# Performance work log

Measured on AMD Instinct MI355X. Metric: run time of the kernel, lower is better.

## Reference

```python
import jax, jax.numpy as jnp
import numpy as np

B, T, D = 64, 512, 512
H = 1024   # hidden_nodes
I = 512    # intermediate_dim
MASK_VALUE = 0.0


def _lstm_layer(x, mask, W, U, b):
    """Keras-style LSTM with return_sequences=True and timestep masking.
    x: [B,T,Din], mask: [B,T] bool, W: [Din,4H], U: [H,4H], b: [4H].
    Gate order (Keras): i, f, g(candidate), o.
    Masked steps carry previous h and c through unchanged.
    """
    Hd = U.shape[0]
    xz = jnp.einsum('btd,dk->btk', x, W) + b          # [B,T,4H] precomputed input projection
    xz_t = jnp.transpose(xz, (1, 0, 2))               # [T,B,4H]
    mask_t = jnp.transpose(mask, (1, 0))              # [T,B]

    def step(carry, inp):
        h, c = carry
        z_in, m = inp
        z = z_in + h @ U                              # [B,4H]
        i, f, g, o = jnp.split(z, 4, axis=-1)
        i = jax.nn.sigmoid(i)
        f = jax.nn.sigmoid(f)
        g = jnp.tanh(g)
        o = jax.nn.sigmoid(o)
        c_new = f * c + i * g
        h_new = o * jnp.tanh(c_new)
        m2 = m[:, None]
        h = jnp.where(m2, h_new, h)
        c = jnp.where(m2, c_new, c)
        return (h, c), h

    h0 = jnp.zeros((x.shape[0], Hd), dtype=x.dtype)
    c0 = jnp.zeros((x.shape[0], Hd), dtype=x.dtype)
    (_, _), hs = jax.lax.scan(step, (h0, c0), (xz_t, mask_t))
    return jnp.transpose(hs, (1, 0, 2))               # [B,T,H]


def setup_inputs() -> dict:
    key = jax.random.key(0)
    ks = jax.random.split(key, 7)
    s = 0.05
    inputs = jax.random.normal(ks[0], (B, T, D), dtype=jnp.float32)
    W0 = jax.random.normal(ks[1], (D, 4 * H), dtype=jnp.float32) * s
    U0 = jax.random.normal(ks[2], (H, 4 * H), dtype=jnp.float32) * s
    b0 = jnp.zeros((4 * H,), dtype=jnp.float32)
    W1 = jax.random.normal(ks[3], (H, 4 * I), dtype=jnp.float32) * s
    U1 = jax.random.normal(ks[4], (I, 4 * I), dtype=jnp.float32) * s
    b1 = jnp.zeros((4 * I,), dtype=jnp.float32)
    return {"inputs": inputs, "W0": W0, "U0": U0, "b0": b0,
            "W1": W1, "U1": U1, "b1": b1}


def reference(inputs, W0, U0, b0, W1, U1, b1):
    # Masking layer: timestep masked if ALL features equal mask_value
    mask = jnp.any(inputs != MASK_VALUE, axis=-1)      # [B,T] bool
    x = _lstm_layer(inputs, mask, W0, U0, b0)          # hidden LSTM, [B,T,H]
    latent = _lstm_layer(x, mask, W1, U1, b1)          # output LSTM, [B,T,I]
    return latent
```

## Files before the change

### kernel.cpp

```cpp
#include <hip/hip_runtime.h>
#include <hip/hip_bf16.h>
#include <cstdint>
#include <cstddef>

#define B_   64
#define T_   512
#define D_   512
#define H0_  1024
#define H1_  512
#define NGRP 4
#define BPG  64
#define NWORK 256

typedef __attribute__((ext_vector_type(8))) short bf16x8;
typedef __attribute__((ext_vector_type(4))) float f32x4;
typedef unsigned long long u64;

#define LDS_ZP0 0
#define LDS_ZP1 17408
#define LDS_BYTES 26624
#define ZROW0 68
#define ZROW1 36

__device__ __forceinline__ float sigmf(float x) { return 1.0f / (1.0f + __expf(-x)); }
__device__ __forceinline__ unsigned short bf16bits(float x) {
    union { __hip_bfloat16 h; unsigned short s; } u; u.h = __float2bfloat16(x); return u.s;
}

__global__ void mask_kernel(const float* __restrict__ x, unsigned char* __restrict__ mask) {
    int row  = blockIdx.x * 4 + (threadIdx.x >> 6);
    int lane = threadIdx.x & 63;
    const float4* p = reinterpret_cast<const float4*>(x + (size_t)row * D_) + lane * 2;
    float4 a = p[0], b = p[1];
    bool nz = (a.x != 0.f) | (a.y != 0.f) | (a.z != 0.f) | (a.w != 0.f)
            | (b.x != 0.f) | (b.y != 0.f) | (b.z != 0.f) | (b.w != 0.f);
    int m = __any(nz);
    if (lane == 0) mask[row] = m ? 1 : 0;
}

__global__ void xbf_kernel(const float* __restrict__ in, __hip_bfloat16* __restrict__ xbf) {
    int i  = blockIdx.x * 256 + threadIdx.x;
    int d8 = i & 63;
    int row = i >> 6;
    int b = row >> 9, t = row & 511;
    const float* src = in + (size_t)row * D_ + d8 * 8;
    __hip_bfloat16 o[8];
    #pragma unroll
    for (int j = 0; j < 8; ++j) o[j] = __float2bfloat16(src[j]);
    *reinterpret_cast<bf16x8*>(xbf + ((size_t)t * B_ + b) * D_ + d8 * 8) =
        *reinterpret_cast<bf16x8*>(o);
}

__global__ __launch_bounds__(256, 1)
void lstm_persistent(const __hip_bfloat16* __restrict__ xbf,
    const float* __restrict__ W0, const float* __restrict__ U0,
    const float* __restrict__ W1, const float* __restrict__ U1,
    const float* __restrict__ b0, const float* __restrict__ b1,
    const unsigned char* __restrict__ mask,
    __hip_bfloat16* h0ring, __hip_bfloat16* h1ring, float* __restrict__ out,
    int* flags)
{
    __shared__ __align__(16) unsigned char smem[LDS_BYTES];
    const int bid = blockIdx.x;
    const int g   = bid >> 6;
    const int lb  = bid & 63;
    const int tid = threadIdx.x;
    const int w = tid >> 6, lane = tid & 63;
    const int mr = lane & 15, kgrp = lane >> 4;
    const int ub0 = lb * 16, ub1 = lb * 8;
    const int brow = g * 16;
    int* gflags = flags + g * BPG;

    bf16x8 bw0[4][4], bu0r[8][4], bw1r[8][2], bu1[4][2];
    {
        const int nn0 = lane & 15;
        #pragma unroll
        for (int c = 0; c < 4; ++c)
            #pragma unroll
            for (int nf = 0; nf < 4; ++nf) {
                int col = nf * 1024 + ub0 + nn0;
                int kb  = (w * 4 + c) * 32 + kgrp * 8;
                union { short s[8]; bf16x8 v; } t;
                #pragma unroll
                for (int j = 0; j < 8; ++j)
                    t.s[j] = (short)bf16bits(W0[(size_t)(kb + j) * 4096 + col]);
                bw0[c][nf] = t.v;
            }
        #pragma unroll
        for (int c = 0; c < 8; ++c)
            #pragma unroll
            for (int nf = 0; nf < 4; ++nf) {
                int col = nf * 1024 + ub0 + nn0;
                int kb  = (w * 8 + c) * 32 + kgrp * 8;
                union { short s[8]; bf16x8 v; } t;
                #pragma unroll
                for (int j = 0; j < 8; ++j)
                    t.s[j] = (short)bf16bits(U0[(size_t)(kb + j) * 4096 + col]);
                bu0r[c][nf] = t.v;
            }
        #pragma unroll
        for (int c = 0; c < 8; ++c)
            #pragma unroll
            for (int nf = 0; nf < 2; ++nf) {
                int nn  = nf * 16 + nn0;
                int col = (nn >> 3) * 512 + ub1 + (nn & 7);
                int kb  = (w * 8 + c) * 32 + kgrp * 8;
                union { short s[8]; bf16x8 v; } t;
                #pragma unroll
                for (int j = 0; j < 8; ++j)
                    t.s[j] = (short)bf16bits(W1[(size_t)(kb + j) * 2048 + col]);
                bw1r[c][nf] = t.v;
            }
        #pragma unroll
        for (int c = 0; c < 4; ++c)
            #pragma unroll
            for (int nf = 0; nf < 2; ++nf) {
                int nn  = nf * 16 + nn0;
                int col = (nn >> 3) * 512 + ub1 + (nn & 7);
                int kb  = (w * 4 + c) * 32 + kgrp * 8;
                union { short s[8]; bf16x8 v; } t;
                #pragma unroll
                for (int j = 0; j < 8; ++j)
                    t.s[j] = (short)bf16bits(U1[(size_t)(kb + j) * 2048 + col]);
                bu1[c][nf] = t.v;
            }
    }

    const bool g0t = (tid < 128);
    const bool g1t = (tid >= 128 && tid < 192);
    const int b0i = tid >> 3;
    const int up0 = (tid & 7) * 2;
    const int b1i = (tid - 128) >> 2;
    const int up1 = ((tid - 128) & 3) * 2;

    float h0reg[2] = {0.f, 0.f}, c0reg[2] = {0.f, 0.f}, br0[8];
    float h1reg[2] = {0.f, 0.f}, c1reg[2] = {0.f, 0.f}, br1[8];
    if (g0t) {
        #pragma unroll
        for (int gg = 0; gg < 4; ++gg) {
            br0[gg]     = b0[gg * H0_ + ub0 + up0];
            br0[4 + gg] = b0[gg * H0_ + ub0 + up0 + 1];
        }
    }
    if (g1t) {
        #pragma unroll
        for (int gg = 0; gg < 4; ++gg) {
            br1[gg]     = b1[gg * H1_ + ub1 + up1];
            br1[4 + gg] = b1[gg * H1_ + ub1 + up1 + 1];
        }
    }
    __syncthreads();

    float* zp0 = (float*)(smem + LDS_ZP0);
    float* zp1 = (float*)(smem + LDS_ZP1);

    #pragma unroll 1
    for (int p = 0; p <= T_; ++p) {
        const bool doL0 = (p < T_);
        const bool doL1 = (p >= 1);

        f32x4 acc0[4];
        f32x4 acc1[2];
        #pragma unroll
        for (int nf = 0; nf < 4; ++nf) { f32x4 z = {0.f,0.f,0.f,0.f}; acc0[nf] = z; }
        #pragma unroll
        for (int nf = 0; nf < 2; ++nf) { f32x4 z = {0.f,0.f,0.f,0.f}; acc1[nf] = z; }

        bool msk0 = false, msk1 = false;
        if (doL0 && g0t) msk0 = mask[(brow + b0i) * T_ + p] != 0;
        if (doL1 && g1t) msk1 = mask[(brow + b1i) * T_ + (p - 1)] != 0;
        if (doL0) {
            const __hip_bfloat16* xa = xbf + (size_t)p * (B_ * D_)
                                     + (size_t)(brow + mr) * D_ + kgrp * 8;
            #pragma unroll
            for (int c = 0; c < 4; ++c) {
                bf16x8 af = *(const bf16x8*)(xa + (w * 4 + c) * 32);
                #pragma unroll
                for (int nf = 0; nf < 4; ++nf)
                    acc0[nf] = __builtin_amdgcn_mfma_f32_16x16x32_bf16(af, bw0[c][nf], acc0[nf], 0, 0, 0);
            }
        }

        if (p > 0) {
            if (tid < 64) {
                for (;;) {
                    int a = __hip_atomic_load(gflags + tid, __ATOMIC_RELAXED, __HIP_MEMORY_SCOPE_AGENT);
                    if (__all(a >= p)) break;
                    __builtin_amdgcn_s_sleep(1);
                }
                __builtin_amdgcn_fence(__ATOMIC_ACQUIRE, "agent");
            }
            __syncthreads();
        }

        const __hip_bfloat16* h0r = h0ring + (size_t)((p + 1) & 1) * (B_ * H0_);
        const __hip_bfloat16* h1r = h1ring + (size_t)(p & 1) * (B_ * H1_);

        bf16x8 h1a[4];
        if (doL1) {
            const __hip_bfloat16* src = h1r + (size_t)(brow + mr) * H1_ + kgrp * 8;
            #pragma unroll
            for (int c = 0; c < 4; ++c)
                h1a[c] = *(const bf16x8*)(src + (w * 4 + c) * 32);
        }

        const __hip_bfloat16* h0s = h0r + (size_t)(brow + mr) * H0_ + kgrp * 8;
        bf16x8 areg[4];
        #pragma unroll
        for (int c = 0; c < 4; ++c)
            areg[c] = *(const bf16x8*)(h0s + (w * 8 + c) * 32);

        if (doL1) {
            #pragma unroll
            for (int c = 0; c < 4; ++c)
                #pragma unroll
                for (int nf = 0; nf < 2; ++nf)
                    acc1[nf] = __builtin_amdgcn_mfma_f32_16x16x32_bf16(h1a[c], bu1[c][nf], acc1[nf], 0, 0, 0);
        }

        #pragma unroll
        for (int c = 0; c < 8; ++c) {
            bf16x8 cur = areg[c & 3];
            if (c + 4 < 8) areg[c & 3] = *(const bf16x8*)(h0s + (w * 8 + c + 4) * 32);
            if (doL0) {
                #pragma unroll
                for (int nf = 0; nf < 4; ++nf)
                    acc0[nf] = __builtin_amdgcn_mfma_f32_16x16x32_bf16(cur, bu0r[c][nf], acc0[nf], 0, 0, 0);
            }
            if (doL1) {
                #pragma unroll
                for (int nf = 0; nf < 2; ++nf)
                    acc1[nf] = __builtin_amdgcn_mfma_f32_16x16x32_bf16(cur, bw1r[c][nf], acc1[nf], 0, 0, 0);
            }
        }

        if (doL0) {
            #pragma unroll
            for (int nf = 0; nf < 4; ++nf)
                #pragma unroll
                for (int r = 0; r < 4; ++r)
                    zp0[(w * 16 + kgrp * 4 + r) * ZROW0 + nf * 16 + mr] = acc0[nf][r];
        }
        if (doL1) {
            #pragma unroll
            for (int nf = 0; nf < 2; ++nf)
                #pragma unroll
                for (int r = 0; r < 4; ++r)
                    zp1[(w * 16 + kgrp * 4 + r) * ZROW1 + nf * 16 + mr] = acc1[nf][r];
        }
        __syncthreads();

        if (doL0 && g0t) {
            float z[2][4];
            #pragma unroll
            for (int gg = 0; gg < 4; ++gg) {
                float sx = 0.f, sy = 0.f;
                #pragma unroll
                for (int wv = 0; wv < 4; ++wv) {
                    float2 s = *(const float2*)&zp0[(wv * 16 + b0i) * ZROW0 + gg * 16 + up0];
                    sx += s.x; sy += s.y;
                }
                z[0][gg] = sx + br0[gg];
                z[1][gg] = sy + br0[4 + gg];
            }
            #pragma unroll
            for (int i = 0; i < 2; ++i) {
                float ig = sigmf(z[i][0]), fg = sigmf(z[i][1]);
                float gv = tanhf(z[i][2]), og = sigmf(z[i][3]);
                float cn = fg * c0reg[i] + ig * gv;
                float hn = og * tanhf(cn);
                if (msk0) { c0reg[i] = cn; h0reg[i] = hn; }
            }
            __hip_bfloat16* h0w = h0ring + (size_t)(p & 1) * (B_ * H0_);
            union { unsigned short s[2]; unsigned u; } hv;
            hv.s[0] = bf16bits(h0reg[0]);
            hv.s[1] = bf16bits(h0reg[1]);
            __hip_atomic_store((unsigned*)&h0w[(size_t)(brow + b0i) * H0_ + ub0 + up0], hv.u,
                               __ATOMIC_RELAXED, __HIP_MEMORY_SCOPE_AGENT);
        }
        if (doL1 && g1t) {
            float z[2][4];
            #pragma unroll
            for (int gg = 0; gg < 4; ++gg) {
                float sx = 0.f, sy = 0.f;
                #pragma unroll
                for (int wv = 0; wv < 4; ++wv) {
                    float2 s = *(const float2*)&zp1[(wv * 16 + b1i) * ZROW1 + gg * 8 + up1];
                    sx += s.x; sy += s.y;
                }
                z[0][gg] = sx + br1[gg];
                z[1][gg] = sy + br1[4 + gg];
            }
            #pragma unroll
            for (int i = 0; i < 2; ++i) {
                float ig = sigmf(z[i][0]), fg = sigmf(z[i][1]);
                float gv = tanhf(z[i][2]), og = sigmf(z[i][3]);
                float cn = fg * c1reg[i] + ig * gv;
                float hn = og * tanhf(cn);
                if (msk1) { c1reg[i] = cn; h1reg[i] = hn; }
            }
            __hip_bfloat16* h1w = h1ring + (size_t)((p + 1) & 1) * (B_ * H1_);
            union { unsigned short s[2]; unsigned u; } hv;
            hv.s[0] = bf16bits(h1reg[0]);
            hv.s[1] = bf16bits(h1reg[1]);
            __hip_atomic_store((unsigned*)&h1w[(size_t)(brow + b1i) * H1_ + ub1 + up1], hv.u,
                               __ATOMIC_RELAXED, __HIP_MEMORY_SCOPE_AGENT);
        }

        __syncthreads();
        if (p < T_ && tid == 0)
            __hip_atomic_store(gflags + lb, p + 1,
                               __ATOMIC_RELAXED, __HIP_MEMORY_SCOPE_AGENT);

        if (doL1 && g1t) {
            const int t1 = p - 1;
            float2 ov; ov.x = h1reg[0]; ov.y = h1reg[1];
            *reinterpret_cast<float2*>(&out[((size_t)(brow + b1i) * T_ + t1) * H1_ + ub1 + up1]) = ov;
        }
    }
}

extern "C" void kernel_launch(void* const* d_in, const int* in_sizes, int n_in,
                              void* d_out, int out_size, void* d_ws, size_t ws_size,
                              hipStream_t stream)
{
    const float* inputs = (const float*)d_in[0];
    const float* W0     = (const float*)d_in[1];
    const float* U0     = (const float*)d_in[2];
    const float* b0     = (const float*)d_in[3];
    const float* W1     = (const float*)d_in[4];
    const float* U1     = (const float*)d_in[5];
    const float* b1     = (const float*)d_in[6];
    float* out = (float*)d_out;

    __hip_bfloat16* xbf    = (__hip_bfloat16*)d_ws;
    __hip_bfloat16* h0ring = xbf + 16777216;
    __hip_bfloat16* h1ring = h0ring + 131072;
    unsigned char*  mask   = (unsigned char*)(h1ring + 65536);
    int* flags = (int*)(mask + 32768);

    hipMemsetAsync(h0ring, 0, (131072 + 65536) * sizeof(__hip_bfloat16), stream);
    hipMemsetAsync(flags, 0, NWORK * sizeof(int), stream);
    mask_kernel<<<(B_ * T_) / 4, 256, 0, stream>>>(inputs, mask);
    xbf_kernel<<<(B_ * T_ * D_ / 8) / 256, 256, 0, stream>>>(inputs, xbf);

    lstm_persistent<<<dim3(NWORK), dim3(256), 0, stream>>>(
        xbf, W0, U0, W1, U1, b0, b1, mask, h0ring, h1ring, out, flags);
}
```

Before: 3.012 ms.

## Use per-wave completion flags and fast sigmoid/tanh in persistent LSTM

Each wave now publishes its own progress flag right after draining its own global stores, which removes the block-wide barrier before the flag store. Waiters poll four flags per block with 64-bit atomic loads. Sigmoid and tanh now use hardware reciprocal and exp-based approximations instead of the library tanhf. The cost is four times as many flags to poll and slightly lower activation accuracy. Memory ordering now relies on each wave's own s_waitcnt before its store.

Measured after the change: 3.157 ms. 4.8% more time.

```diff
diff --git a/kernel.cpp b/kernel.cpp
--- a/kernel.cpp
+++ b/kernel.cpp
@@ -22,9 +22,19 @@
 #define ZROW0 68
 #define ZROW1 36
 
-__device__ __forceinline__ float sigmf(float x) { return 1.0f / (1.0f + __expf(-x)); }
+__device__ __forceinline__ float sigmf(float x) {
+    return __builtin_amdgcn_rcpf(1.0f + __expf(-x));
+}
+__device__ __forceinline__ float ftanh(float x) {
+    float xc = fminf(fmaxf(x, -15.f), 15.f);
+    float t = __expf(2.f * xc);
+    return (t - 1.f) * __builtin_amdgcn_rcpf(t + 1.f);
+}
 __device__ __forceinline__ unsigned short bf16bits(float x) {
     union { __hip_bfloat16 h; unsigned short s; } u; u.h = __float2bfloat16(x); return u.s;
+}
+__device__ __forceinline__ u64 ald(const void* p) {
+    return __hip_atomic_load((const u64*)p, __ATOMIC_RELAXED, __HIP_MEMORY_SCOPE_AGENT);
 }
 
 __global__ void mask_kernel(const float* __restrict__ x, unsigned char* __restrict__ mask) {
@@ -69,7 +79,7 @@
     const int mr = lane & 15, kgrp = lane >> 4;
     const int ub0 = lb * 16, ub1 = lb * 8;
     const int brow = g * 16;
-    int* gflags = flags + g * BPG;
+    int* gflags = flags + g * (BPG * 4);
 
     bf16x8 bw0[4][4], bu0r[8][4], bw1r[8][2], bu1[4][2];
     {
@@ -183,9 +193,13 @@
 
         if (p > 0) {
             if (tid < 64) {
+                const u64* f = (const u64*)gflags + tid;
                 for (;;) {
-                    int a = __hip_atomic_load(gflags + tid, __ATOMIC_RELAXED, __HIP_MEMORY_SCOPE_AGENT);
-                    if (__all(a >= p)) break;
+                    u64 a = ald(f);
+                    u64 b = ald(f + 64);
+                    bool ok = ((int)a >= p) && ((int)(a >> 32) >= p)
+                           && ((int)b >= p) && ((int)(b >> 32) >= p);
+                    if (__all(ok)) break;
                     __builtin_amdgcn_s_sleep(1);
                 }
                 __builtin_amdgcn_fence(__ATOMIC_ACQUIRE, "agent");
@@ -266,9 +280,9 @@
             #pragma unroll
             for (int i = 0; i < 2; ++i) {
                 float ig = sigmf(z[i][0]), fg = sigmf(z[i][1]);
-                float gv = tanhf(z[i][2]), og = sigmf(z[i][3]);
+                float gv = ftanh(z[i][2]), og = sigmf(z[i][3]);
                 float cn = fg * c0reg[i] + ig * gv;
-                float hn = og * tanhf(cn);
+                float hn = og * ftanh(cn);
                 if (msk0) { c0reg[i] = cn; h0reg[i] = hn; }
             }
             __hip_bfloat16* h0w = h0ring + (size_t)(p & 1) * (B_ * H0_);
@@ -294,9 +308,9 @@
             #pragma unroll
             for (int i = 0; i < 2; ++i) {
                 float ig = sigmf(z[i][0]), fg = sigmf(z[i][1]);
-                float gv = tanhf(z[i][2]), og = sigmf(z[i][3]);
+                float gv = ftanh(z[i][2]), og = sigmf(z[i][3]);
                 float cn = fg * c1reg[i] + ig * gv;
-                float hn = og * tanhf(cn);
+                float hn = og * ftanh(cn);
                 if (msk1) { c1reg[i] = cn; h1reg[i] = hn; }
             }
             __hip_bfloat16* h1w = h1ring + (size_t)((p + 1) & 1) * (B_ * H1_);
@@ -307,10 +321,12 @@
                                __ATOMIC_RELAXED, __HIP_MEMORY_SCOPE_AGENT);
         }
 
-        __syncthreads();
-        if (p < T_ && tid == 0)
-            __hip_atomic_store(gflags + lb, p + 1,
-                               __ATOMIC_RELAXED, __HIP_MEMORY_SCOPE_AGENT);
+        if (p < T_) {
+            asm volatile("s_waitcnt vmcnt(0)" ::: "memory");
+            if (lane == 0)
+                __hip_atomic_store(gflags + lb * 4 + w, p + 1,
+                                   __ATOMIC_RELAXED, __HIP_MEMORY_SCOPE_AGENT);
+        }
 
         if (doL1 && g1t) {
             const int t1 = p - 1;
@@ -340,7 +356,7 @@
     int* flags = (int*)(mask + 32768);
 
     hipMemsetAsync(h0ring, 0, (131072 + 65536) * sizeof(__hip_bfloat16), stream);
-    hipMemsetAsync(flags, 0, NWORK * sizeof(int), stream);
+    hipMemsetAsync(flags, 0, NGRP * BPG * 4 * sizeof(int), stream);
     mask_kernel<<<(B_ * T_) / 4, 256, 0, stream>>>(inputs, mask);
     xbf_kernel<<<(B_ * T_ * D_ / 8) / 256, 256, 0, stream>>>(inputs, xbf);
 
```
